# Kernel tuning notes

Hardware: AMD Instinct MI355X
Metric: run time of the kernel (lower is better)

## Reference

```python
import jax, jax.numpy as jnp
import numpy as np

N = 100000   # nodes
E = 200000   # edges
D = 512      # in_features
H = 512      # out_features


def setup_inputs() -> dict:
    key = jax.random.key(0)
    ks = jax.random.split(key, 12)
    s = 0.04  # ~1/sqrt(512), keeps gates out of saturation like nn.Linear init
    rng = np.random.default_rng(0)
    edge_index = jnp.asarray(rng.integers(0, N, size=(2, E)), dtype=jnp.int32)
    return {
        "x": jax.random.normal(ks[0], (N, D), jnp.float32),
        "edge_index": edge_index,
        "edge_feats": jax.random.normal(ks[1], (10, D), jnp.float32),
        "edge_types": jax.random.uniform(ks[2], (E, 10), jnp.float32),
        "W_iou_w": jax.random.normal(ks[3], (3 * H, D), jnp.float32) * s,
        "W_iou_b": jax.random.normal(ks[4], (3 * H,), jnp.float32) * s,
        "U_iou_w": jax.random.normal(ks[5], (3 * H, H), jnp.float32) * s,
        "U_iou_b": jax.random.normal(ks[6], (3 * H,), jnp.float32) * s,
        "W_f_w": jax.random.normal(ks[7], (H, D), jnp.float32) * s,
        "W_f_b": jax.random.normal(ks[8], (H,), jnp.float32) * s,
        "U_f_w": jax.random.normal(ks[9], (H, H), jnp.float32) * s,
        "U_f_b": jax.random.normal(ks[10], (H,), jnp.float32) * s,
    }


def _orders(parents, n_nodes):
    """node_order[p] = #edges with parent p; edge_order[i] = 1-based rank of edge i
    among same-parent edges in edge-list order (matches the torch python loop)."""
    e = parents.shape[0]
    node_order = np.zeros(n_nodes, dtype=np.int64)
    np.add.at(node_order, parents, 1)
    order = np.argsort(parents, kind="stable")
    sp = parents[order]
    is_new = np.ones(e, dtype=bool)
    is_new[1:] = sp[1:] != sp[:-1]
    pos = np.arange(e)
    start = pos[is_new][np.cumsum(is_new) - 1]  # start index of each parent group
    edge_order = np.zeros(e, dtype=np.int64)
    edge_order[order] = pos - start + 1
    return node_order, edge_order


def reference(x, edge_index, edge_feats, edge_types, W_iou_w, W_iou_b,
              U_iou_w, U_iou_b, W_f_w, W_f_b, U_f_w, U_f_b):
    # edge_feats / edge_types are unused in the default (untyped) path, as in the torch code.
    ei = np.asarray(edge_index)
    parents, children = ei[0], ei[1]
    n_nodes = x.shape[0]
    out_f = W_f_b.shape[0]
    node_order, edge_order = _orders(parents, n_nodes)
    max_iter = int(node_order.max()) if parents.size else 0

    h = jnp.zeros((n_nodes, out_f), x.dtype)
    c = jnp.zeros((n_nodes, out_f), x.dtype)
    h_sum = jnp.zeros((n_nodes, out_f), x.dtype)

    for n in range(max_iter + 1):
        nm = np.nonzero(node_order == n)[0]       # nodes evaluated this wavefront
        xn = x[nm]
        if n == 0:
            iou = xn @ W_iou_w.T + W_iou_b
        else:
            em = np.nonzero(edge_order == n)[0]   # n-th child edge of each parent
            p, ch = parents[em], children[em]     # p is unique within a wavefront
            child_h = h[ch]
            child_c = c[ch]
            h_sum = h_sum.at[p].add(child_h)
            iou = xn @ W_iou_w.T + W_iou_b + h_sum[nm] @ U_iou_w.T + U_iou_b
        i, o, u = jnp.split(iou, 3, axis=1)
        i, o, u = jax.nn.sigmoid(i), jax.nn.sigmoid(o), jnp.tanh(u)
        c = c.at[nm].set(i * u)
        if n > 0:
            f = jax.nn.sigmoid(x[p] @ W_f_w.T + W_f_b + child_h @ U_f_w.T + U_f_b)
            c = c.at[p].add(f * child_c)
        h = h.at[nm].set(o * jnp.tanh(c[nm]))
    return h
```

## Files before the change

### kernel.cpp

```cpp
#include <hip/hip_runtime.h>
#include <math.h>

#define MAXIT 16
#define MAXDEG 16

typedef __attribute__((ext_vector_type(8))) short bf16x8;
typedef __attribute__((ext_vector_type(16))) float f32x16;

static inline int imin(int a, int b) { return a < b ? a : b; }

__device__ __forceinline__ float sigm(float v) { return 1.0f / (1.0f + __expf(-v)); }
__device__ __forceinline__ float tfast(float v) {
  float vc = fminf(fmaxf(v, -20.0f), 20.0f);
  float t = __expf(2.0f * vc);
  return (t - 1.0f) / (t + 1.0f);
}
__device__ __forceinline__ unsigned short f2bf(float f) {
  unsigned int u = __float_as_uint(f);
  u += 0x7FFFu + ((u >> 16) & 1u);
  return (unsigned short)(u >> 16);
}
__device__ __forceinline__ float bf2f(unsigned short s) {
  return __uint_as_float(((unsigned int)s) << 16);
}
__device__ __forceinline__ unsigned bfadd2(unsigned x, unsigned y) {
  float sl = bf2f((unsigned short)(x & 0xFFFFu)) + bf2f((unsigned short)(y & 0xFFFFu));
  float sh = bf2f((unsigned short)(x >> 16)) + bf2f((unsigned short)(y >> 16));
  return (unsigned)f2bf(sl) | ((unsigned)f2bf(sh) << 16);
}
__device__ __forceinline__ uint4 bfadd8(uint4 a, uint4 b) {
  return make_uint4(bfadd2(a.x, b.x), bfadd2(a.y, b.y), bfadd2(a.z, b.z), bfadd2(a.w, b.w));
}

__global__ void kzero16(uint4* p, size_t n) {
  size_t i = (size_t)blockIdx.x * blockDim.x + threadIdx.x;
  size_t st = (size_t)gridDim.x * blockDim.x;
  uint4 z = make_uint4(0u, 0u, 0u, 0u);
  for (; i < n; i += st) p[i] = z;
}
__global__ void kzeroi(int* p, int n) {
  int i = blockIdx.x * blockDim.x + threadIdx.x;
  if (i < n) p[i] = 0;
}
__global__ void kfill(float* p, size_t n, float v) {
  size_t i = (size_t)blockIdx.x * blockDim.x + threadIdx.x;
  size_t st = (size_t)gridDim.x * blockDim.x;
  for (; i < n; i += st) p[i] = v;
}

__global__ void k_histo(const int* __restrict__ par, int E,
                        int* __restrict__ node_order, int* __restrict__ bucket) {
  int e = blockIdx.x * blockDim.x + threadIdx.x;
  if (e >= E) return;
  int p = par[e];
  int slot = atomicAdd(&node_order[p], 1);
  if (slot < MAXDEG) bucket[(size_t)p * MAXDEG + slot] = e;
}

__global__ void k_rank(const int* __restrict__ par, int E, int N,
                       const int* __restrict__ node_order, const int* __restrict__ bucket,
                       int* __restrict__ edgeCnt, int* __restrict__ edgeList) {
  __shared__ int lcnt[MAXIT], lbase[MAXIT];
  const int t = threadIdx.x;
  if (t < MAXIT) lcnt[t] = 0;
  __syncthreads();
  int e = blockIdx.x * blockDim.x + t;
  int r = 0, ls = 0;
  if (e < E) {
    int p = par[e];
    int d = node_order[p]; if (d > MAXDEG) d = MAXDEG;
    int rr = 1;
    for (int j = 0; j < d; ++j) rr += (bucket[(size_t)p * MAXDEG + j] < e) ? 1 : 0;
    if (rr < MAXIT) { r = rr; ls = atomicAdd(&lcnt[rr], 1); }
  }
  __syncthreads();
  if (t < MAXIT && lcnt[t] > 0) lbase[t] = atomicAdd(&edgeCnt[t], lcnt[t]);
  __syncthreads();
  if (r > 0) edgeList[(size_t)r * N + lbase[r] + ls] = e;
}

__global__ void k_nodelist(int N, const int* __restrict__ node_order,
                           int* __restrict__ nodeCnt, int* __restrict__ nodeList) {
  __shared__ int lcnt[MAXIT], lbase[MAXIT];
  const int t = threadIdx.x;
  if (t < MAXIT) lcnt[t] = 0;
  __syncthreads();
  int v = blockIdx.x * blockDim.x + t;
  int n = -1, ls = 0;
  if (v < N) {
    n = node_order[v]; if (n >= MAXIT) n = MAXIT - 1;
    ls = atomicAdd(&lcnt[n], 1);
  }
  __syncthreads();
  if (t < MAXIT && lcnt[t] > 0) lbase[t] = atomicAdd(&nodeCnt[t], lcnt[t]);
  __syncthreads();
  if (n >= 0) nodeList[(size_t)n * N + lbase[n] + ls] = v;
}

__global__ void k_pack_x(const float* __restrict__ x, unsigned short* __restrict__ xb, size_t n8) {
  size_t i = (size_t)blockIdx.x * blockDim.x + threadIdx.x;
  size_t st = (size_t)gridDim.x * blockDim.x;
  for (; i < n8; i += st) {
    const float* p = x + i * 8;
    float4 f0 = *(const float4*)p, f1 = *(const float4*)(p + 4);
    uint4 r;
    r.x = (unsigned)f2bf(f0.x) | ((unsigned)f2bf(f0.y) << 16);
    r.y = (unsigned)f2bf(f0.z) | ((unsigned)f2bf(f0.w) << 16);
    r.z = (unsigned)f2bf(f1.x) | ((unsigned)f2bf(f1.y) << 16);
    r.w = (unsigned)f2bf(f1.z) | ((unsigned)f2bf(f1.w) << 16);
    *(uint4*)(xb + i * 8) = r;
  }
}

__global__ void k_pack_biou(const float* __restrict__ W, const float* __restrict__ U,
                            unsigned short* __restrict__ Bpk) {
  int i = blockIdx.x * blockDim.x + threadIdx.x;
  if (i >= 16 * 64 * 3 * 64) return;
  int lane = i & 63;
  int q = i >> 6;
  int g = q % 3; q /= 3;
  int s = q & 63;
  int jc = q >> 6;
  int col = jc * 32 + (lane & 31);
  int k0 = s * 16 + (lane >> 5) * 8;
  int rowW = g * 512 + col;
  unsigned short v[8];
#pragma unroll
  for (int j = 0; j < 8; ++j) {
    int kk = k0 + j;
    v[j] = f2bf(kk < 512 ? W[(size_t)rowW * 512 + kk] : U[(size_t)rowW * 512 + kk - 512]);
  }
  *(uint4*)(Bpk + (size_t)i * 8) = *(uint4*)v;
}

__global__ void k_pack_bf(const float* __restrict__ W, const float* __restrict__ U,
                          unsigned short* __restrict__ Bpk) {
  int i = blockIdx.x * blockDim.x + threadIdx.x;
  if (i >= 16 * 64 * 64) return;
  int lane = i & 63;
  int q = i >> 6;
  int s = q & 63;
  int jc = q >> 6;
  int col = jc * 32 + (lane & 31);
  int k0 = s * 16 + (lane >> 5) * 8;
  unsigned short v[8];
#pragma unroll
  for (int j = 0; j < 8; ++j) {
    int kk = k0 + j;
    v[j] = f2bf(kk < 512 ? W[(size_t)col * 512 + kk] : U[(size_t)col * 512 + kk - 512]);
  }
  *(uint4*)(Bpk + (size_t)i * 8) = *(uint4*)v;
}

__global__ void k_pack_u3(const float* __restrict__ U, unsigned short* __restrict__ Bpk) {
  int i = blockIdx.x * blockDim.x + threadIdx.x;
  if (i >= 16 * 32 * 3 * 64) return;
  int lane = i & 63;
  int q = i >> 6;
  int g = q % 3; q /= 3;
  int s = q & 31;
  int jc = q >> 5;
  int col = jc * 32 + (lane & 31);
  int k0 = s * 16 + (lane >> 5) * 8;
  int rowW = g * 512 + col;
  unsigned short v[8];
#pragma unroll
  for (int j = 0; j < 8; ++j) v[j] = f2bf(U[(size_t)rowW * 512 + k0 + j]);
  *(uint4*)(Bpk + (size_t)i * 8) = *(uint4*)v;
}

__global__ void k_pack_uf(const float* __restrict__ U, unsigned short* __restrict__ Bpk) {
  int i = blockIdx.x * blockDim.x + threadIdx.x;
  if (i >= 16 * 32 * 64) return;
  int lane = i & 63;
  int q = i >> 6;
  int s = q & 31;
  int jc = q >> 5;
  int col = jc * 32 + (lane & 31);
  int k0 = s * 16 + (lane >> 5) * 8;
  unsigned short v[8];
#pragma unroll
  for (int j = 0; j < 8; ++j) v[j] = f2bf(U[(size_t)col * 512 + k0 + j]);
  *(uint4*)(Bpk + (size_t)i * 8) = *(uint4*)v;
}

__global__ void k_pack_wx(const float* __restrict__ Wiou, const float* __restrict__ Wf,
                          unsigned short* __restrict__ Bpk) {
  int i = blockIdx.x * blockDim.x + threadIdx.x;
  if (i >= 64 * 32 * 64) return;
  int lane = i & 63;
  int q = i >> 6;
  int s = q & 31;
  int jc = q >> 5;
  int col = jc * 32 + (lane & 31);
  int k0 = s * 16 + (lane >> 5) * 8;
  const float* src = (col < 1536) ? (Wiou + (size_t)col * 512)
                                  : (Wf + (size_t)(col - 1536) * 512);
  unsigned short v[8];
#pragma unroll
  for (int j = 0; j < 8; ++j) v[j] = f2bf(src[k0 + j]);
  *(uint4*)(Bpk + (size_t)i * 8) = *(uint4*)v;
}

__global__ void k_edge_pre(int n, int N, const int* __restrict__ edgeCnt, const int* __restrict__ edgeList,
                           const int* __restrict__ par, const int* __restrict__ chd,
                           const int* __restrict__ node_order,
                           const unsigned short* __restrict__ hb, unsigned short* __restrict__ hsumb,
                           const unsigned short* __restrict__ fc, float* __restrict__ c) {
  const int cntH = edgeCnt[n];
  const int cntA = (n >= 2) ? edgeCnt[n - 1] : 0;
  const size_t totH = (size_t)cntH * 64;
  const size_t total = totH + (size_t)cntA * 64;
  size_t st = (size_t)gridDim.x * blockDim.x;
  for (size_t i = (size_t)blockIdx.x * blockDim.x + threadIdx.x; i < total; i += st) {
    if (i < totH) {
      int slot = (int)(i >> 6), j8 = ((int)i & 63) << 3;
      int e = edgeList[(size_t)n * N + slot];
      int p = par[e], ch = chd[e];
      uint4 hv = *(const uint4*)&hb[(size_t)ch * 512 + j8];
      if (n == 1) {
        *(uint4*)&hsumb[(size_t)p * 512 + j8] = hv;
      } else {
        uint4 hs = *(const uint4*)&hsumb[(size_t)p * 512 + j8];
        *(uint4*)&hsumb[(size_t)p * 512 + j8] = bfadd8(hs, hv);
      }
    } else {
      size_t k = i - totH;
      int slot = (int)(k >> 6), j8 = ((int)k & 63) << 3;
      int e = edgeList[(size_t)(n - 1) * N + slot];
      int p = par[e];
      if (node_order[p] <= n - 1) continue;
      size_t base = (size_t)p * 512 + j8;
      uint4 f8 = *(const uint4*)&fc[base];
      unsigned fw[4] = {f8.x, f8.y, f8.z, f8.w};
      float4 c0 = *(const float4*)&c[base];
      float4 c1 = *(const float4*)&c[base + 4];
      c0.x += bf2f((unsigned short)(fw[0] & 0xFFFFu)); c0.y += bf2f((unsigned short)(fw[0] >> 16));
      c0.z += bf2f((unsigned short)(fw[1] & 0xFFFFu)); c0.w += bf2f((unsigned short)(fw[1] >> 16));
      c1.x += bf2f((unsigned short)(fw[2] & 0xFFFFu)); c1.y += bf2f((unsigned short)(fw[2] >> 16));
      c1.z += bf2f((unsigned short)(fw[3] & 0xFFFFu)); c1.w += bf2f((unsigned short)(fw[3] >> 16));
      *(float4*)&c[base] = c0;
      *(float4*)&c[base + 4] = c1;
    }
  }
}

template<int MODE>
__global__ __launch_bounds__(256, 2)
void k_gemm9(int n, int N, const int* __restrict__ cntArr, const int* __restrict__ list,
             const int* __restrict__ par, const int* __restrict__ chd,
             const unsigned short* __restrict__ xb, const unsigned short* __restrict__ hsrc,
             const unsigned short* __restrict__ Bpk,
             const float* __restrict__ bW, const float* __restrict__ bU,
             float* __restrict__ c, float* __restrict__ h, unsigned short* __restrict__ hb,
             unsigned short* __restrict__ fc) {
  const int cnt = cntArr[n];
  if (cnt == 0) return;
  constexpr int KS    = (MODE == 0) ? 32 : 64;
  constexpr int KC8   = KS * 2;
  constexpr int GATES = (MODE == 2) ? 1 : 3;
  constexpr int NSTR  = (MODE == 2) ? 2 : 1;
  constexpr int NPASS = (MODE == 2) ? 2 : 4;
  constexpr int D     = 4;
  const int rowTiles = (cnt + 31) >> 5;

  __shared__ uint4 lA4[KS * 64];
  __shared__ int ids0[32], ids1[32];
  const int t = threadIdx.x, lane = t & 63, w = t >> 6;

  auto ldA = [&](int s) -> bf16x8 {
    int hk = lane >> 5, rl = lane & 31;
    return *(const bf16x8*)&lA4[s * 64 + hk * 32 + (rl ^ ((2 * s + hk) & 31))];
  };

  for (int tile = blockIdx.x; tile < rowTiles; tile += gridDim.x) {
    __syncthreads();
    if (t < 32) {
      int r = (tile << 5) + t;
      int idx = (r < cnt) ? list[(size_t)n * N + r] : -1;
      if (MODE == 2) { ids0[t] = idx >= 0 ? par[idx] : -1; ids1[t] = idx >= 0 ? chd[idx] : 0; }
      else           { ids0[t] = idx; ids1[t] = 0; }
    }
    __syncthreads();

    constexpr int ITERS = (32 * KC8) / 256;
#pragma unroll
    for (int i = 0; i < ITERS; ++i) {
      int cid = i * 256 + t;
      int row = cid >> ((MODE == 0) ? 6 : 7);
      int kc8 = cid & (KC8 - 1);
      int id0 = ids0[row];
      int id = id0 < 0 ? 0 : id0;
      uint4 v;
      if (MODE == 0 || kc8 < 64) {
        v = *(const uint4*)(xb + (size_t)id * 512 + (kc8 << 3));
      } else {
        int idh = (MODE == 2) ? ids1[row] : id;
        v = *(const uint4*)(hsrc + (size_t)idh * 512 + ((kc8 - 64) << 3));
      }
      int s = kc8 >> 1, hk = kc8 & 1;
      lA4[s * 64 + hk * 32 + (row ^ (kc8 & 31))] = v;
    }
    __syncthreads();

    for (int p = 0; p < NPASS; ++p) {
      const uint4* bb[NSTR];
#pragma unroll
      for (int str = 0; str < NSTR; ++str) {
        int jc = (MODE == 2) ? (p * 8 + str * 4 + w) : (p * 4 + w);
        bb[str] = (const uint4*)Bpk + (size_t)jc * 64 * GATES * 64 + lane;
      }
      f32x16 acc[NSTR][GATES];
#pragma unroll
      for (int str = 0; str < NSTR; ++str)
#pragma unroll
        for (int g = 0; g < GATES; ++g)
#pragma unroll
          for (int q = 0; q < 16; ++q) acc[str][g][q] = 0.f;

      bf16x8 aP[D];
      uint4 bP[D][NSTR * GATES];
#pragma unroll
      for (int d = 0; d < D; ++d) {
        aP[d] = ldA(d);
#pragma unroll
        for (int str = 0; str < NSTR; ++str)
#pragma unroll
          for (int g = 0; g < GATES; ++g)
            bP[d][str * GATES + g] = bb[str][(size_t)(d * GATES + g) * 64];
      }
      for (int s0 = 0; s0 < KS - D; s0 += D) {
#pragma unroll
        for (int d = 0; d < D; ++d) {
#pragma unroll
          for (int str = 0; str < NSTR; ++str)
#pragma unroll
            for (int g = 0; g < GATES; ++g)
              acc[str][g] = __builtin_amdgcn_mfma_f32_32x32x16_bf16(
                  aP[d], *(bf16x8*)&bP[d][str * GATES + g], acc[str][g], 0, 0, 0);
          aP[d] = ldA(s0 + D + d);
#pragma unroll
          for (int str = 0; str < NSTR; ++str)
#pragma unroll
            for (int g = 0; g < GATES; ++g)
              bP[d][str * GATES + g] = bb[str][(size_t)((s0 + D + d) * GATES + g) * 64];
        }
      }
#pragma unroll
      for (int d = 0; d < D; ++d)
#pragma unroll
        for (int str = 0; str < NSTR; ++str)
#pragma unroll
          for (int g = 0; g < GATES; ++g)
            acc[str][g] = __builtin_amdgcn_mfma_f32_32x32x16_bf16(
                aP[d], *(bf16x8*)&bP[d][str * GATES + g], acc[str][g], 0, 0, 0);

#pragma unroll
      for (int str = 0; str < NSTR; ++str) {
        const int jc = (MODE == 2) ? (p * 8 + str * 4 + w) : (p * 4 + w);
        const int jh = jc * 32 + (lane & 31);
        if (MODE < 2) {
          float bi = bW[jh], bo = bW[512 + jh], bu = bW[1024 + jh];
          if (MODE == 1) { bi += bU[jh]; bo += bU[512 + jh]; bu += bU[1024 + jh]; }
#pragma unroll
          for (int reg = 0; reg < 16; ++reg) {
            int rl = ((lane >> 5) << 2) + (reg & 3) + ((reg >> 2) << 3);
            int node = ids0[rl];
            if (node < 0) continue;
            size_t base = (size_t)node * 512 + jh;
            float iv = acc[str][0][reg] + bi;
            float ov = acc[str][1][reg] + bo;
            float uv = acc[str][2][reg] + bu;
            float fcv = (MODE == 1) ? bf2f(fc[base]) : 0.f;
            float cn = sigm(iv) * tfast(uv) + fcv;
            c[base] = cn;
            float hv = sigm(ov) * tfast(cn);
            h[base] = hv;
            hb[base] = f2bf(hv);
          }
        } else {
          float bfv = bW[jh] + bU[jh];
#pragma unroll
          for (int reg = 0; reg < 16; ++reg) {
            int rl = ((lane >> 5) << 2) + (reg & 3) + ((reg >> 2) << 3);
            int pe = ids0[rl];
            if (pe < 0) continue;
            int ce = ids1[rl];
            float fv = sigm(acc[str][0][reg] + bfv);
            fc[(size_t)pe * 512 + jh] = f2bf(fv * c[(size_t)ce * 512 + jh]);
          }
        }
      }
    }
  }
}

__global__ __launch_bounds__(256, 2)
void k_pxiou(int N, const float* __restrict__ x, const unsigned short* __restrict__ BpkX,
             unsigned short* __restrict__ px) {
  const int rowTiles = (N + 31) >> 5;
  __shared__ uint4 lA4[32 * 64];
  const int t = threadIdx.x, lane = t & 63, w = t >> 6;

  auto ldA = [&](int s) -> bf16x8 {
    int hk = lane >> 5, rl = lane & 31;
    return *(const bf16x8*)&lA4[s * 64 + hk * 32 + (rl ^ ((2 * s + hk) & 31))];
  };

  for (int tile = blockIdx.x; tile < rowTiles; tile += gridDim.x) {
    __syncthreads();
#pragma unroll
    for (int i = 0; i < 8; ++i) {
      int cid = i * 256 + t;
      int row = cid >> 6;
      int kc8 = cid & 63;
      int grow = (tile << 5) + row;
      if (grow >= N) grow = N - 1;
      const float* p = x + (size_t)grow * 512 + (kc8 << 3);
      float4 f0 = *(const float4*)p, f1 = *(const float4*)(p + 4);
      uint4 v;
      v.x = (unsigned)f2bf(f0.x) | ((unsigned)f2bf(f0.y) << 16);
      v.y = (unsigned)f2bf(f0.z) | ((unsigned)f2bf(f0.w) << 16);
      v.z = (unsigned)f2bf(f1.x) | ((unsigned)f2bf(f1.y) << 16);
      v.w = (unsigned)f2bf(f1.z) | ((unsigned)f2bf(f1.w) << 16);
      int s = kc8 >> 1, hk = kc8 & 1;
      lA4[s * 64 + hk * 32 + (row ^ (kc8 & 31))] = v;
    }
    __syncthreads();

    for (int p = 0; p < 16; ++p) {
      const int jc = p * 4 + w;
      const uint4* bb = (const uint4*)BpkX + (size_t)jc * 32 * 64 + lane;
      f32x16 acc;
#pragma unroll
      for (int q = 0; q < 16; ++q) acc[q] = 0.f;
      bf16x8 aP[4];
      uint4 bP[4];
#pragma unroll
      for (int d = 0; d < 4; ++d) { aP[d] = ldA(d); bP[d] = bb[(size_t)d * 64]; }
      for (int s0 = 0; s0 < 28; s0 += 4) {
#pragma unroll
        for (int d = 0; d < 4; ++d) {
          acc = __builtin_amdgcn_mfma_f32_32x32x16_bf16(aP[d], *(bf16x8*)&bP[d], acc, 0, 0, 0);
          aP[d] = ldA(s0 + 4 + d);
          bP[d] = bb[(size_t)(s0 + 4 + d) * 64];
        }
      }
#pragma unroll
      for (int d = 0; d < 4; ++d)
        acc = __builtin_amdgcn_mfma_f32_32x32x16_bf16(aP[d], *(bf16x8*)&bP[d], acc, 0, 0, 0);

      const int jh = jc * 32 + (lane & 31);
#pragma unroll
      for (int reg = 0; reg < 16; ++reg) {
        int rl = ((lane >> 5) << 2) + (reg & 3) + ((reg >> 2) << 3);
        int grow = (tile << 5) + rl;
        if (grow < N) px[(size_t)grow * 2048 + jh] = f2bf(acc[reg]);
      }
    }
  }
}

__global__ void k_wave0(int N, const int* __restrict__ nodeCnt, const int* __restrict__ nodeList,
                        const unsigned short* __restrict__ px, const float* __restrict__ bW,
                        float* __restrict__ c, float* __restrict__ h, unsigned short* __restrict__ hb) {
  size_t total = (size_t)nodeCnt[0] * 512;
  size_t st = (size_t)gridDim.x * blockDim.x;
  for (size_t i = (size_t)blockIdx.x * blockDim.x + threadIdx.x; i < total; i += st) {
    int slot = (int)(i >> 9), col = (int)(i & 511);
    int node = nodeList[slot];
    size_t pb = (size_t)node * 2048;
    float iv = bf2f(px[pb + col]) + bW[col];
    float ov = bf2f(px[pb + 512 + col]) + bW[512 + col];
    float uv = bf2f(px[pb + 1024 + col]) + bW[1024 + col];
    float cn = sigm(iv) * tfast(uv);
    size_t base = (size_t)node * 512 + col;
    c[base] = cn;
    float hv = sigm(ov) * tfast(cn);
    h[base] = hv;
    hb[base] = f2bf(hv);
  }
}

template<int MODE>
__global__ __launch_bounds__(256, 2)
void k_gemmS(int n, int N, const int* __restrict__ cntArr, const int* __restrict__ list,
             const int* __restrict__ par, const int* __restrict__ chd,
             const unsigned short* __restrict__ asrc, const unsigned short* __restrict__ Bpk,
             const unsigned short* __restrict__ px,
             const float* __restrict__ bW, const float* __restrict__ bU,
             float* __restrict__ c, float* __restrict__ h, unsigned short* __restrict__ hb,
             unsigned short* __restrict__ fc) {
  const int cnt = cntArr[n];
  if (cnt == 0) return;
  constexpr int KS    = 32;
  constexpr int GATES = (MODE == 2) ? 1 : 3;
  constexpr int NSTR  = (MODE == 2) ? 2 : 1;
  constexpr int NPASS = (MODE == 2) ? 2 : 4;
  constexpr int D     = 4;
  const int rowTiles = (cnt + 31) >> 5;

  __shared__ uint4 lA4[KS * 64];
  __shared__ int ids0[32], ids1[32];
  const int t = threadIdx.x, lane = t & 63, w = t >> 6;

  auto ldA = [&](int s) -> bf16x8 {
    int hk = lane >> 5, rl = lane & 31;
    return *(const bf16x8*)&lA4[s * 64 + hk * 32 + (rl ^ ((2 * s + hk) & 31))];
  };

  for (int tile = blockIdx.x; tile < rowTiles; tile += gridDim.x) {
    __syncthreads();
    if (t < 32) {
      int r = (tile << 5) + t;
      int idx = (r < cnt) ? list[(size_t)n * N + r] : -1;
      if (MODE == 2) { ids0[t] = idx >= 0 ? par[idx] : -1; ids1[t] = idx >= 0 ? chd[idx] : 0; }
      else           { ids0[t] = idx; ids1[t] = 0; }
    }
    __syncthreads();

#pragma unroll
    for (int i = 0; i < 8; ++i) {
      int cid = i * 256 + t;
      int row = cid >> 6;
      int kc8 = cid & 63;
      int id = (MODE == 2) ? ids1[row] : ids0[row];
      if (id < 0) id = 0;
      uint4 v = *(const uint4*)(asrc + (size_t)id * 512 + (kc8 << 3));
      int s = kc8 >> 1, hk = kc8 & 1;
      lA4[s * 64 + hk * 32 + (row ^ (kc8 & 31))] = v;
    }
    __syncthreads();

    for (int p = 0; p < NPASS; ++p) {
      const uint4* bb[NSTR];
#pragma unroll
      for (int str = 0; str < NSTR; ++str) {
        int jc = (MODE == 2) ? (p * 8 + str * 4 + w) : (p * 4 + w);
        bb[str] = (const uint4*)Bpk + (size_t)jc * KS * GATES * 64 + lane;
      }
      f32x16 acc[NSTR][GATES];
#pragma unroll
      for (int str = 0; str < NSTR; ++str)
#pragma unroll
        for (int g = 0; g < GATES; ++g)
#pragma unroll
          for (int q = 0; q < 16; ++q) acc[str][g][q] = 0.f;

      bf16x8 aP[D];
      uint4 bP[D][NSTR * GATES];
#pragma unroll
      for (int d = 0; d < D; ++d) {
        aP[d] = ldA(d);
#pragma unroll
        for (int str = 0; str < NSTR; ++str)
#pragma unroll
          for (int g = 0; g < GATES; ++g)
            bP[d][str * GATES + g] = bb[str][(size_t)(d * GATES + g) * 64];
      }
      for (int s0 = 0; s0 < KS - D; s0 += D) {
#pragma unroll
        for (int d = 0; d < D; ++d) {
#pragma unroll
          for (int str = 0; str < NSTR; ++str)
#pragma unroll
            for (int g = 0; g < GATES; ++g)
              acc[str][g] = __builtin_amdgcn_mfma_f32_32x32x16_bf16(
                  aP[d], *(bf16x8*)&bP[d][str * GATES + g], acc[str][g], 0, 0, 0);
          aP[d] = ldA(s0 + D + d);
#pragma unroll
          for (int str = 0; str < NSTR; ++str)
#pragma unroll
            for (int g = 0; g < GATES; ++g)
              bP[d][str * GATES + g] = bb[str][(size_t)((s0 + D + d) * GATES + g) * 64];
        }
      }
#pragma unroll
      for (int d = 0; d < D; ++d)
#pragma unroll
        for (int str = 0; str < NSTR; ++str)
#pragma unroll
          for (int g = 0; g < GATES; ++g)
            acc[str][g] = __builtin_amdgcn_mfma_f32_32x32x16_bf16(
                aP[d], *(bf16x8*)&bP[d][str * GATES + g], acc[str][g], 0, 0, 0);

#pragma unroll
      for (int str = 0; str < NSTR; ++str) {
        const int jc = (MODE == 2) ? (p * 8 + str * 4 + w) : (p * 4 + w);
        const int jh = jc * 32 + (lane & 31);
        if (MODE == 1) {
          float bi = bW[jh] + bU[jh];
          float bo = bW[512 + jh] + bU[512 + jh];
          float bu = bW[1024 + jh] + bU[1024 + jh];
#pragma unroll
          for (int reg = 0; reg < 16; ++reg) {
            int rl = ((lane >> 5) << 2) + (reg & 3) + ((reg >> 2) << 3);
            int node = ids0[rl];
            if (node < 0) continue;
            size_t base = (size_t)node * 512 + jh;
            size_t pb = (size_t)node * 2048;
            float iv = acc[str][0][reg] + bf2f(px[pb + jh]) + bi;
            float ov = acc[str][1][reg] + bf2f(px[pb + 512 + jh]) + bo;
            float uv = acc[str][2][reg] + bf2f(px[pb + 1024 + jh]) + bu;
            float fcv = bf2f(fc[base]);
            float cn = sigm(iv) * tfast(uv) + fcv;
            c[base] = cn;
            float hv = sigm(ov) * tfast(cn);
            h[base] = hv;
            hb[base] = f2bf(hv);
          }
        } else {
          float bfv = bW[jh] + bU[jh];
#pragma unroll
          for (int reg = 0; reg < 16; ++reg) {
            int rl = ((lane >> 5) << 2) + (reg & 3) + ((reg >> 2) << 3);
            int pe = ids0[rl];
            if (pe < 0) continue;
            int ce = ids1[rl];
            float fv = sigm(acc[str][0][reg] + bf2f(px[(size_t)pe * 2048 + 1536 + jh]) + bfv);
            fc[(size_t)pe * 512 + jh] = f2bf(fv * c[(size_t)ce * 512 + jh]);
          }
        }
      }
    }
  }
}

static void run_allA(const float* x, const int* par, const int* chd,
                     const float* Wiou, const float* bWiou, const float* Uiou, const float* bUiou,
                     const float* Wf, const float* bWf, const float* Uf, const float* bUf,
                     float* h, int N, int E, void* d_ws, hipStream_t stream) {
  const size_t NV = (size_t)N * 512;
  char* cur = (char*)d_ws;
  auto take = [&](size_t bytes) -> char* {
    char* r = cur; cur += (bytes + 255) & ~(size_t)255; return r;
  };
  float* c             = (float*)take(NV * 4);
  unsigned short* hb   = (unsigned short*)take(NV * 2);
  unsigned short* hsumb= (unsigned short*)take(NV * 2);
  unsigned short* fc   = (unsigned short*)take(NV * 2);
  unsigned short* px   = (unsigned short*)take((size_t)N * 2048 * 2);
  unsigned short* BpkU3= (unsigned short*)take((size_t)16 * 32 * 3 * 64 * 8 * 2);
  unsigned short* BpkUF= (unsigned short*)take((size_t)16 * 32 * 64 * 8 * 2);
  unsigned short* BpkX = (unsigned short*)take((size_t)64 * 32 * 64 * 8 * 2);
  int* node_order      = (int*)take((size_t)N * 4);
  int* nodeCnt         = (int*)take(MAXIT * 4);
  int* edgeCnt         = (int*)take(MAXIT * 4);
  int* bucket          = (int*)take((size_t)N * MAXDEG * 4);
  int* nodeList        = (int*)take((size_t)MAXIT * N * 4);
  int* edgeList        = (int*)take((size_t)MAXIT * N * 4);

  kzero16<<<2048, 256, 0, stream>>>((uint4*)c, NV * 4 / 16);
  kzero16<<<2048, 256, 0, stream>>>((uint4*)hb, NV * 2 / 16);
  kzeroi<<<(N + 255) / 256, 256, 0, stream>>>(node_order, N);
  kzeroi<<<1, 64, 0, stream>>>(nodeCnt, MAXIT);
  kzeroi<<<1, 64, 0, stream>>>(edgeCnt, MAXIT);

  k_pack_u3<<<(16 * 32 * 3 * 64 + 255) / 256, 256, 0, stream>>>(Uiou, BpkU3);
  k_pack_uf<<<(16 * 32 * 64 + 255) / 256, 256, 0, stream>>>(Uf, BpkUF);
  k_pack_wx<<<(64 * 32 * 64 + 255) / 256, 256, 0, stream>>>(Wiou, Wf, BpkX);

  k_histo<<<(E + 255) / 256, 256, 0, stream>>>(par, E, node_order, bucket);
  k_rank<<<(E + 255) / 256, 256, 0, stream>>>(par, E, N, node_order, bucket, edgeCnt, edgeList);
  k_nodelist<<<(N + 255) / 256, 256, 0, stream>>>(N, node_order, nodeCnt, nodeList);

  k_pxiou<<<imin(4096, (N + 31) >> 5), 256, 0, stream>>>(N, x, BpkX, px);
  k_wave0<<<2048, 256, 0, stream>>>(N, nodeCnt, nodeList, px, bWiou, c, h, hb);

  for (int n = 1; n < MAXIT; ++n) {
    int boundE = E / n;
    int boundN = imin(N, boundE);
    int boundA = (n >= 2) ? (E / (n - 1)) : 0;
    int gE = imin(2048, (int)(((size_t)(boundE + boundA) * 64 + 255) / 256));
    int gF = imin(4096, (boundE + 31) >> 5);
    int gI = imin(4096, (boundN + 31) >> 5);
    k_edge_pre<<<gE, 256, 0, stream>>>(n, N, edgeCnt, edgeList, par, chd, node_order,
                                       hb, hsumb, fc, c);
    k_gemmS<2><<<gF, 256, 0, stream>>>(n, N, edgeCnt, edgeList, par, chd,
                                       hb, BpkUF, px, bWf, bUf, c, h, hb, fc);
    k_gemmS<1><<<gI, 256, 0, stream>>>(n, N, nodeCnt, nodeList, par, chd,
                                       hsumb, BpkU3, px, bWiou, bUiou, c, h, hb, fc);
  }
}

static void run_allB(const float* x, const int* par, const int* chd,
                     const float* Wiou, const float* bWiou, const float* Uiou, const float* bUiou,
                     const float* Wf, const float* bWf, const float* Uf, const float* bUf,
                     float* h, int N, int E, void* d_ws, hipStream_t stream) {
  const size_t NV = (size_t)N * 512;
  char* cur = (char*)d_ws;
  auto take = [&](size_t bytes) -> char* {
    char* r = cur; cur += (bytes + 255) & ~(size_t)255; return r;
  };
  float* c             = (float*)take(NV * 4);
  unsigned short* hb   = (unsigned short*)take(NV * 2);
  unsigned short* hsumb= (unsigned short*)take(NV * 2);
  unsigned short* xb   = (unsigned short*)take(NV * 2);
  unsigned short* fc   = (unsigned short*)take(NV * 2);
  unsigned short* BpkI = (unsigned short*)take((size_t)16 * 64 * 3 * 64 * 8 * 2);
  unsigned short* BpkF = (unsigned short*)take((size_t)16 * 64 * 64 * 8 * 2);
  int* node_order      = (int*)take((size_t)N * 4);
  int* nodeCnt         = (int*)take(MAXIT * 4);
  int* edgeCnt         = (int*)take(MAXIT * 4);
  int* bucket          = (int*)take((size_t)N * MAXDEG * 4);
  int* nodeList        = (int*)take((size_t)MAXIT * N * 4);
  int* edgeList        = (int*)take((size_t)MAXIT * N * 4);

  kzero16<<<2048, 256, 0, stream>>>((uint4*)c, NV * 4 / 16);
  kzero16<<<2048, 256, 0, stream>>>((uint4*)hb, NV * 2 / 16);
  kzeroi<<<(N + 255) / 256, 256, 0, stream>>>(node_order, N);
  kzeroi<<<1, 64, 0, stream>>>(nodeCnt, MAXIT);
  kzeroi<<<1, 64, 0, stream>>>(edgeCnt, MAXIT);

  k_pack_x<<<2048, 256, 0, stream>>>(x, xb, NV / 8);
  k_pack_biou<<<(16 * 64 * 3 * 64 + 255) / 256, 256, 0, stream>>>(Wiou, Uiou, BpkI);
  k_pack_bf<<<(16 * 64 * 64 + 255) / 256, 256, 0, stream>>>(Wf, Uf, BpkF);

  k_histo<<<(E + 255) / 256, 256, 0, stream>>>(par, E, node_order, bucket);
  k_rank<<<(E + 255) / 256, 256, 0, stream>>>(par, E, N, node_order, bucket, edgeCnt, edgeList);
  k_nodelist<<<(N + 255) / 256, 256, 0, stream>>>(N, node_order, nodeCnt, nodeList);

  {
    int g = imin(4096, (N + 31) >> 5);
    k_gemm9<0><<<g, 256, 0, stream>>>(0, N, nodeCnt, nodeList, par, chd,
                                      xb, hsumb, BpkI, bWiou, bUiou, c, h, hb, fc);
  }
  for (int n = 1; n < MAXIT; ++n) {
    int boundE = E / n;
    int boundN = imin(N, boundE);
    int boundA = (n >= 2) ? (E / (n - 1)) : 0;
    int gE = imin(2048, (int)(((size_t)(boundE + boundA) * 64 + 255) / 256));
    int gF = imin(4096, (boundE + 31) >> 5);
    int gI = imin(4096, (boundN + 31) >> 5);
    k_edge_pre<<<gE, 256, 0, stream>>>(n, N, edgeCnt, edgeList, par, chd, node_order,
                                       hb, hsumb, fc, c);
    k_gemm9<2><<<gF, 256, 0, stream>>>(n, N, edgeCnt, edgeList, par, chd,
                                       xb, hb, BpkF, bWf, bUf, c, h, hb, fc);
    k_gemm9<1><<<gI, 256, 0, stream>>>(n, N, nodeCnt, nodeList, par, chd,
                                       xb, hsumb, BpkI, bWiou, bUiou, c, h, hb, fc);
  }
}

extern "C" void kernel_launch(void* const* d_in, const int* in_sizes, int n_in,
                              void* d_out, int out_size, void* d_ws, size_t ws_size,
                              hipStream_t stream) {
  (void)n_in; (void)out_size;
  const float* x     = (const float*)d_in[0];
  const int*   ei    = (const int*)d_in[1];
  const float* Wiou  = (const float*)d_in[4];
  const float* bWiou = (const float*)d_in[5];
  const float* Uiou  = (const float*)d_in[6];
  const float* bUiou = (const float*)d_in[7];
  const float* Wf    = (const float*)d_in[8];
  const float* bWf   = (const float*)d_in[9];
  const float* Uf    = (const float*)d_in[10];
  const float* bUf   = (const float*)d_in[11];
  const int N = in_sizes[0] / 512;
  const int E = in_sizes[1] / 2;
  const int* par = ei;
  const int* chd = ei + E;
  float* h = (float*)d_out;

  const size_t NV = (size_t)N * 512;
  const size_t ints = ((size_t)N * (1 + MAXDEG + 2 * MAXIT) + 256) * 4;
  const size_t needA = NV * 18 + (size_t)8 * 1024 * 1024 + ints;
  const size_t needB = NV * 12 + (size_t)8 * 1024 * 1024 + ints;

  if (ws_size >= needA) {
    run_allA(x, par, chd, Wiou, bWiou, Uiou, bUiou, Wf, bWf, Uf, bUf,
             h, N, E, d_ws, stream);
  } else if (ws_size >= needB) {
    run_allB(x, par, chd, Wiou, bWiou, Uiou, bUiou, Wf, bWf, Uf, bUf,
             h, N, E, d_ws, stream);
  } else {
    kfill<<<2048, 256, 0, stream>>>(h, NV, 1.0e6f);
  }
}
```

Before: 2.625 ms.

## Split projection buffer and alias forget-gate projections into output buffer

The x-projection kernel now computes two 32-column output strips per warp, so each LDS A-fragment load feeds two MFMAs instead of one. Its results are written to two buffers instead of one interleaved 2048-wide array: a 1536-wide iou buffer in the workspace, and the 512-wide forget-gate projection stored in the output h buffer. That aliasing is safe only because each node's f-projection row is last read before that node's h row is written. It shrinks the workspace requirement for path A, so the faster path can be chosen with less scratch memory. The cost is more register pressure from the doubled accumulators and a fragile dependence on kernel ordering.

```diff
diff --git a/kernel.cpp b/kernel.cpp
--- a/kernel.cpp
+++ b/kernel.cpp
@@ -396,8 +396,8 @@
 }
 
 __global__ __launch_bounds__(256, 2)
-void k_pxiou(int N, const float* __restrict__ x, const unsigned short* __restrict__ BpkX,
-             unsigned short* __restrict__ px) {
+void k_pxall(int N, const float* __restrict__ x, const unsigned short* __restrict__ BpkX,
+             unsigned short* __restrict__ pxIou, unsigned short* __restrict__ pxF) {
   const int rowTiles = (N + 31) >> 5;
   __shared__ uint4 lA4[32 * 64];
   const int t = threadIdx.x, lane = t & 63, w = t >> 6;
@@ -428,51 +428,75 @@
     }
     __syncthreads();
 
-    for (int p = 0; p < 16; ++p) {
-      const int jc = p * 4 + w;
-      const uint4* bb = (const uint4*)BpkX + (size_t)jc * 32 * 64 + lane;
-      f32x16 acc;
-#pragma unroll
-      for (int q = 0; q < 16; ++q) acc[q] = 0.f;
+    for (int p = 0; p < 8; ++p) {
+      const uint4* bb[2];
+#pragma unroll
+      for (int str = 0; str < 2; ++str) {
+        int jc = p * 8 + str * 4 + w;
+        bb[str] = (const uint4*)BpkX + (size_t)jc * 32 * 64 + lane;
+      }
+      f32x16 acc[2];
+#pragma unroll
+      for (int str = 0; str < 2; ++str)
+#pragma unroll
+        for (int q = 0; q < 16; ++q) acc[str][q] = 0.f;
+
       bf16x8 aP[4];
-      uint4 bP[4];
-#pragma unroll
-      for (int d = 0; d < 4; ++d) { aP[d] = ldA(d); bP[d] = bb[(size_t)d * 64]; }
+      uint4 bP[4][2];
+#pragma unroll
+      for (int d = 0; d < 4; ++d) {
+        aP[d] = ldA(d);
+#pragma unroll
+        for (int str = 0; str < 2; ++str) bP[d][str] = bb[str][(size_t)d * 64];
+      }
       for (int s0 = 0; s0 < 28; s0 += 4) {
 #pragma unroll
         for (int d = 0; d < 4; ++d) {
-          acc = __builtin_amdgcn_mfma_f32_32x32x16_bf16(aP[d], *(bf16x8*)&bP[d], acc, 0, 0, 0);
+#pragma unroll
+          for (int str = 0; str < 2; ++str)
+            acc[str] = __builtin_amdgcn_mfma_f32_32x32x16_bf16(
+                aP[d], *(bf16x8*)&bP[d][str], acc[str], 0, 0, 0);
           aP[d] = ldA(s0 + 4 + d);
-          bP[d] = bb[(size_t)(s0 + 4 + d) * 64];
+#pragma unroll
+          for (int str = 0; str < 2; ++str) bP[d][str] = bb[str][(size_t)(s0 + 4 + d) * 64];
         }
       }
 #pragma unroll
       for (int d = 0; d < 4; ++d)
-        acc = __builtin_amdgcn_mfma_f32_32x32x16_bf16(aP[d], *(bf16x8*)&bP[d], acc, 0, 0, 0);
-
-      const int jh = jc * 32 + (lane & 31);
-#pragma unroll
-      for (int reg = 0; reg < 16; ++reg) {
-        int rl = ((lane >> 5) << 2) + (reg & 3) + ((reg >> 2) << 3);
-        int grow = (tile << 5) + rl;
-        if (grow < N) px[(size_t)grow * 2048 + jh] = f2bf(acc[reg]);
+#pragma unroll
+        for (int str = 0; str < 2; ++str)
+          acc[str] = __builtin_amdgcn_mfma_f32_32x32x16_bf16(
+              aP[d], *(bf16x8*)&bP[d][str], acc[str], 0, 0, 0);
+
+#pragma unroll
+      for (int str = 0; str < 2; ++str) {
+        const int jh = (p * 8 + str * 4 + w) * 32 + (lane & 31);
+#pragma unroll
+        for (int reg = 0; reg < 16; ++reg) {
+          int rl = ((lane >> 5) << 2) + (reg & 3) + ((reg >> 2) << 3);
+          int grow = (tile << 5) + rl;
+          if (grow >= N) continue;
+          unsigned short bv = f2bf(acc[str][reg]);
+          if (jh < 1536) pxIou[(size_t)grow * 1536 + jh] = bv;
+          else           pxF[(size_t)grow * 1024 + (jh - 1536)] = bv;
+        }
       }
     }
   }
 }
 
 __global__ void k_wave0(int N, const int* __restrict__ nodeCnt, const int* __restrict__ nodeList,
-                        const unsigned short* __restrict__ px, const float* __restrict__ bW,
+                        const unsigned short* __restrict__ pxIou, const float* __restrict__ bW,
                         float* __restrict__ c, float* __restrict__ h, unsigned short* __restrict__ hb) {
   size_t total = (size_t)nodeCnt[0] * 512;
   size_t st = (size_t)gridDim.x * blockDim.x;
   for (size_t i = (size_t)blockIdx.x * blockDim.x + threadIdx.x; i < total; i += st) {
     int slot = (int)(i >> 9), col = (int)(i & 511);
     int node = nodeList[slot];
-    size_t pb = (size_t)node * 2048;
-    float iv = bf2f(px[pb + col]) + bW[col];
-    float ov = bf2f(px[pb + 512 + col]) + bW[512 + col];
-    float uv = bf2f(px[pb + 1024 + col]) + bW[1024 + col];
+    size_t pb = (size_t)node * 1536;
+    float iv = bf2f(pxIou[pb + col]) + bW[col];
+    float ov = bf2f(pxIou[pb + 512 + col]) + bW[512 + col];
+    float uv = bf2f(pxIou[pb + 1024 + col]) + bW[1024 + col];
     float cn = sigm(iv) * tfast(uv);
     size_t base = (size_t)node * 512 + col;
     c[base] = cn;
@@ -487,7 +511,7 @@
 void k_gemmS(int n, int N, const int* __restrict__ cntArr, const int* __restrict__ list,
              const int* __restrict__ par, const int* __restrict__ chd,
              const unsigned short* __restrict__ asrc, const unsigned short* __restrict__ Bpk,
-             const unsigned short* __restrict__ px,
+             const unsigned short* __restrict__ pxIou, const unsigned short* __restrict__ pxF,
              const float* __restrict__ bW, const float* __restrict__ bU,
              float* __restrict__ c, float* __restrict__ h, unsigned short* __restrict__ hb,
              unsigned short* __restrict__ fc) {
@@ -598,10 +622,10 @@
             int node = ids0[rl];
             if (node < 0) continue;
             size_t base = (size_t)node * 512 + jh;
-            size_t pb = (size_t)node * 2048;
-            float iv = acc[str][0][reg] + bf2f(px[pb + jh]) + bi;
-            float ov = acc[str][1][reg] + bf2f(px[pb + 512 + jh]) + bo;
-            float uv = acc[str][2][reg] + bf2f(px[pb + 1024 + jh]) + bu;
+            size_t pb = (size_t)node * 1536;
+            float iv = acc[str][0][reg] + bf2f(pxIou[pb + jh]) + bi;
+            float ov = acc[str][1][reg] + bf2f(pxIou[pb + 512 + jh]) + bo;
+            float uv = acc[str][2][reg] + bf2f(pxIou[pb + 1024 + jh]) + bu;
             float fcv = bf2f(fc[base]);
             float cn = sigm(iv) * tfast(uv) + fcv;
             c[base] = cn;
@@ -617,7 +641,7 @@
             int pe = ids0[rl];
             if (pe < 0) continue;
             int ce = ids1[rl];
-            float fv = sigm(acc[str][0][reg] + bf2f(px[(size_t)pe * 2048 + 1536 + jh]) + bfv);
+            float fv = sigm(acc[str][0][reg] + bf2f(pxF[(size_t)pe * 1024 + jh]) + bfv);
             fc[(size_t)pe * 512 + jh] = f2bf(fv * c[(size_t)ce * 512 + jh]);
           }
         }
@@ -639,7 +663,7 @@
   unsigned short* hb   = (unsigned short*)take(NV * 2);
   unsigned short* hsumb= (unsigned short*)take(NV * 2);
   unsigned short* fc   = (unsigned short*)take(NV * 2);
-  unsigned short* px   = (unsigned short*)take((size_t)N * 2048 * 2);
+  unsigned short* pxI  = (unsigned short*)take((size_t)N * 1536 * 2);
   unsigned short* BpkU3= (unsigned short*)take((size_t)16 * 32 * 3 * 64 * 8 * 2);
   unsigned short* BpkUF= (unsigned short*)take((size_t)16 * 32 * 64 * 8 * 2);
   unsigned short* BpkX = (unsigned short*)take((size_t)64 * 32 * 64 * 8 * 2);
@@ -650,6 +674,8 @@
   int* nodeList        = (int*)take((size_t)MAXIT * N * 4);
   int* edgeList        = (int*)take((size_t)MAXIT * N * 4);
 
+  unsigned short* pxF = (unsigned short*)h;
+
   kzero16<<<2048, 256, 0, stream>>>((uint4*)c, NV * 4 / 16);
   kzero16<<<2048, 256, 0, stream>>>((uint4*)hb, NV * 2 / 16);
   kzeroi<<<(N + 255) / 256, 256, 0, stream>>>(node_order, N);
@@ -664,8 +690,8 @@
   k_rank<<<(E + 255) / 256, 256, 0, stream>>>(par, E, N, node_order, bucket, edgeCnt, edgeList);
   k_nodelist<<<(N + 255) / 256, 256, 0, stream>>>(N, node_order, nodeCnt, nodeList);
 
-  k_pxiou<<<imin(4096, (N + 31) >> 5), 256, 0, stream>>>(N, x, BpkX, px);
-  k_wave0<<<2048, 256, 0, stream>>>(N, nodeCnt, nodeList, px, bWiou, c, h, hb);
+  k_pxall<<<imin(4096, (N + 31) >> 5), 256, 0, stream>>>(N, x, BpkX, pxI, pxF);
+  k_wave0<<<2048, 256, 0, stream>>>(N, nodeCnt, nodeList, pxI, bWiou, c, h, hb);
 
   for (int n = 1; n < MAXIT; ++n) {
     int boundE = E / n;
@@ -677,9 +703,9 @@
     k_edge_pre<<<gE, 256, 0, stream>>>(n, N, edgeCnt, edgeList, par, chd, node_order,
                                        hb, hsumb, fc, c);
     k_gemmS<2><<<gF, 256, 0, stream>>>(n, N, edgeCnt, edgeList, par, chd,
-                                       hb, BpkUF, px, bWf, bUf, c, h, hb, fc);
+                                       hb, BpkUF, pxI, pxF, bWf, bUf, c, h, hb, fc);
     k_gemmS<1><<<gI, 256, 0, stream>>>(n, N, nodeCnt, nodeList, par, chd,
-                                       hsumb, BpkU3, px, bWiou, bUiou, c, h, hb, fc);
+                                       hsumb, BpkU3, pxI, pxF, bWiou, bUiou, c, h, hb, fc);
   }
 }
 
@@ -762,8 +788,8 @@
   float* h = (float*)d_out;
 
   const size_t NV = (size_t)N * 512;
-  const size_t ints = ((size_t)N * (1 + MAXDEG + 2 * MAXIT) + 256) * 4;
-  const size_t needA = NV * 18 + (size_t)8 * 1024 * 1024 + ints;
+  const size_t ints = ((size_t)N * (1 + MAXDEG + 2 * MAXIT) + 512) * 4;
+  const size_t needA = NV * 16 + (size_t)8 * 1024 * 1024 + ints;
   const size_t needB = NV * 12 + (size_t)8 * 1024 * 1024 + ints;
 
   if (ws_size >= needA) {
```

New measurement: 2.621 ms. Within noise of the previous version (-0.2%).
